# Kernel optimization log

Measured on AMD Instinct MI355X. Metric: run time of the kernel, lower is better.

Reference implementation:

```python
import jax, jax.numpy as jnp
import numpy as np

NUM_ENTITIES = 50000
NUM_RELATIONS = 500
DIM = 100
BATCH = 16
EPS = 1e-5  # torch BatchNorm1d default eps


def _bn2(x, gamma, beta):
    # train-mode BatchNorm1d on (B, d): stats over batch axis
    mean = jnp.mean(x, axis=0, keepdims=True)
    var = jnp.var(x, axis=0, keepdims=True)
    return (x - mean) * jax.lax.rsqrt(var + EPS) * gamma + beta


def _bn3(x, gamma, beta):
    # train-mode BatchNorm1d on (B, d, N): stats over (batch, length)
    mean = jnp.mean(x, axis=(0, 2), keepdims=True)
    var = jnp.var(x, axis=(0, 2), keepdims=True)
    return (x - mean) * jax.lax.rsqrt(var + EPS) * gamma[None, :, None] + beta[None, :, None]


def _cmul(a, b):
    return (a[0] * b[0] - a[1] * b[1], a[0] * b[1] + a[1] * b[0])


def _cadd(a, b):
    return (a[0] + b[0], a[1] + b[1])


def _cdiv(a, b):
    den = b[0] * b[0] + b[1] * b[1]
    return ((a[0] * b[0] + a[1] * b[1]) / den, (a[1] * b[0] - a[0] * b[1]) / den)


def setup_inputs() -> dict:
    key = jax.random.key(0)
    ks = jax.random.split(key, 12)
    d = DIM
    inp = {
        "h_idx": jax.random.randint(ks[0], (BATCH,), 0, NUM_ENTITIES),
        "r_idx": jax.random.randint(ks[1], (BATCH,), 0, NUM_RELATIONS),
        # ComplexEmbedding E (real, imag)
        "E_a": jax.random.normal(ks[2], (NUM_ENTITIES, d), jnp.float32) * 0.1,
        "E_b": jax.random.normal(ks[3], (NUM_ENTITIES, d), jnp.float32) * 0.1,
        # MobiusEmbedding R: 4 complex coefficients (a,b,c,d), real/imag parts
        "R_re": jax.random.normal(ks[4], (NUM_RELATIONS, 4, d), jnp.float32) * 0.1,
        "R_im": jax.random.normal(ks[5], (NUM_RELATIONS, 4, d), jnp.float32) * 0.1,
        # plain relation embedding feeding the Tucker cores
        "R2": jax.random.normal(ks[6], (NUM_RELATIONS, d), jnp.float32) * 0.1,
        # Tucker cores (relation_dim, entity_dim, entity_dim)
        "W_re": jax.random.uniform(ks[7], (d, d, d), jnp.float32, -0.1, 0.1),
        "W_im": jax.random.uniform(ks[8], (d, d, d), jnp.float32, -0.1, 0.1),
    }
    # BatchNorm affine params (bn0/bn1 of each CoreTuckER, and complex E_bn)
    gk = jax.random.split(ks[9], 6)
    bk = jax.random.split(ks[10], 6)
    names = ["g0r", "g1r", "g0i", "g1i", "gEa", "gEb"]
    bnames = ["b0r", "b1r", "b0i", "b1i", "bEa", "bEb"]
    for i, (gn, bn) in enumerate(zip(names, bnames)):
        inp[gn] = 1.0 + 0.05 * jax.random.normal(gk[i], (d,), jnp.float32)
        inp[bn] = 0.05 * jax.random.normal(bk[i], (d,), jnp.float32)
    return inp


def _forward(h_idx, r_idx, E_a, E_b, R_re, R_im, R2, W_re, W_im,
             g0r, b0r, g1r, b1r, g0i, b0i, g1i, b1i, gEa, bEa, gEb, bEb):
    h_a = E_a[h_idx]            # (B, d)
    h_b = E_b[h_idx]
    r2 = R2[r_idx]              # (B, d)

    # relation-specific Tucker maps W_mat = r2 . W  -> (B, d, d)
    Wm_re = jnp.einsum("bk,kef->bef", r2, W_re)
    Wm_im = jnp.einsum("bk,kef->bef", r2, W_im)

    def core(h, Wm, g0, b0, g1, b1):
        x = _bn2(h, g0, b0)
        x = jnp.einsum("be,bef->bf", x, Wm)  # (B,1,d) bmm (B,d,d)
        return _bn2(x, g1, b1)

    t_a = core(h_a, Wm_re, g0r, b0r, g1r, b1r)
    t_b = core(h_b, Wm_im, g0i, b0i, g1i, b1i)

    # Mobius multiplication: (h*r_a + r_b) / (h*r_c + r_d)
    rr = R_re[r_idx]            # (B, 4, d)
    ri = R_im[r_idx]
    h = (t_a, t_b)
    r_a = (rr[:, 0], ri[:, 0]); r_b = (rr[:, 1], ri[:, 1])
    r_c = (rr[:, 2], ri[:, 2]); r_d = (rr[:, 3], ri[:, 3])
    top = _cadd(_cmul(h, r_a), r_b)
    bot = _cadd(_cmul(h, r_c), r_d)
    t = _cdiv(top, bot)         # complex pair, each (B, d)

    # transform ALL entities with the same relation-specific Tucker map
    # CoreTuckER.w: (B,e,f) x (N,e) -> (B, f, N)
    Ea_t = jnp.einsum("bef,ne->bfn", Wm_re, E_a)
    Eb_t = jnp.einsum("bef,ne->bfn", Wm_im, E_b)
    # ComplexBatchNorm1d on (B, d, N); dropout is identity in eval mode
    Ea_t = _bn3(Ea_t, gEa, bEa)
    Eb_t = _bn3(Eb_t, gEb, bEb)

    # BatchComplexScoringAll: (B,1,d) bmm (B,d,N) for each complex part
    score = (jnp.einsum("bf,bfn->bn", t[0], Ea_t)
             + jnp.einsum("bf,bfn->bn", t[1], Eb_t))
    return jax.nn.sigmoid(score)  # (B, N)


def reference(h_idx, r_idx, E_a, E_b, R_re, R_im, R2, W_re, W_im,
              g0r, b0r, g1r, b1r, g0i, b0i, g1i, b1i, gEa, bEa, gEb, bEb):
    return _forward(h_idx, r_idx, E_a, E_b, R_re, R_im, R2, W_re, W_im,
                    g0r, b0r, g1r, b1r, g0i, b0i, g1i, b1i, gEa, bEa, gEb, bEb)
```

## Files before the change

### kernel.cpp

```cpp
#include <hip/hip_runtime.h>
#include <math.h>

#define D100 100
#define NE 50000
#define BATCH 16
#define EPS_F 1e-5f
#define TPT 782
#define NB2 196
#define TPB2 4
#define SLICES 16
#define QCI 10
#define QNJ 1664

typedef __attribute__((ext_vector_type(8))) short short8;
typedef __attribute__((ext_vector_type(16))) float float16;
typedef unsigned short u16;

__device__ __forceinline__ u16 f2bf(float x) {
  union { float f; unsigned u; } c; c.f = x;
  unsigned r = c.u + 0x7FFFu + ((c.u >> 16) & 1u);
  return (u16)(r >> 16);
}
__device__ __forceinline__ float bf2f(u16 v) {
  return __uint_as_float(((unsigned)v) << 16);
}
__device__ __forceinline__ float f4get(const float4& v, int j) {
  switch (j) { case 0: return v.x; case 1: return v.y; case 2: return v.z; default: return v.w; }
}

__global__ void k1_wm(const float* __restrict__ W_re, const float* __restrict__ W_im,
                      const float* __restrict__ R2, const int* __restrict__ r_idx,
                      float* __restrict__ Wm) {
  const int t = blockIdx.y;
  const float* W = t ? W_im : W_re;
  int ef = blockIdx.x * 256 + threadIdx.x;
  if (ef >= 10000) return;
  int ridx[16];
#pragma unroll
  for (int b = 0; b < 16; b++) ridx[b] = r_idx[b];
  float acc[16];
#pragma unroll
  for (int b = 0; b < 16; b++) acc[b] = 0.f;
  for (int k = 0; k < 100; k++) {
    float w = W[k * 10000 + ef];
#pragma unroll
    for (int b = 0; b < 16; b++) acc[b] = fmaf(R2[ridx[b] * 100 + k], w, acc[b]);
  }
  float* o = Wm + t * 160000 + ef;
#pragma unroll
  for (int b = 0; b < 16; b++) o[b * 10000] = acc[b];
}

__global__ void k1a_wm(const float* __restrict__ W_re, const float* __restrict__ W_im,
                       const float* __restrict__ R2, const int* __restrict__ r_idx,
                       float* __restrict__ Wm_p) {
  const int t = blockIdx.z, kc = blockIdx.y;
  const float* W = t ? W_im : W_re;
  const float4* W4 = (const float4*)W;
  __shared__ float r2s[16][12];
  const int tid = threadIdx.x;
  for (int i = tid; i < 160; i += 256) {
    int b = i / 10, kk = i - b * 10;
    r2s[b][kk] = R2[r_idx[b] * 100 + kc * 10 + kk];
  }
  __syncthreads();
  int ef4 = blockIdx.x * 256 + tid;
  if (ef4 < 2500) {
    float4 acc[16];
#pragma unroll
    for (int b = 0; b < 16; b++) acc[b] = make_float4(0.f, 0.f, 0.f, 0.f);
#pragma unroll
    for (int kk = 0; kk < 10; kk++) {
      float4 w = W4[(kc * 10 + kk) * 2500 + ef4];
#pragma unroll
      for (int b = 0; b < 16; b++) {
        float r = r2s[b][kk];
        acc[b].x = fmaf(r, w.x, acc[b].x);
        acc[b].y = fmaf(r, w.y, acc[b].y);
        acc[b].z = fmaf(r, w.z, acc[b].z);
        acc[b].w = fmaf(r, w.w, acc[b].w);
      }
    }
    float4* o = (float4*)(Wm_p + (long)kc * 320000 + t * 160000);
#pragma unroll
    for (int b = 0; b < 16; b++) o[b * 2500 + ef4] = acc[b];
  }
}

__global__ void k1b_reduce(const float* __restrict__ Wm_p, float* __restrict__ Wm) {
  int i4 = blockIdx.x * 256 + threadIdx.x;
  if (i4 >= 80000) return;
  const float4* P4 = (const float4*)Wm_p;
  float4 o = make_float4(0.f, 0.f, 0.f, 0.f);
#pragma unroll
  for (int j = 0; j < 10; j++) {
    float4 a = P4[(long)j * 80000 + i4];
    o.x += a.x; o.y += a.y; o.z += a.z; o.w += a.w;
  }
  ((float4*)Wm)[i4] = o;
}

__global__ __launch_bounds__(256) void k2f_gram(const float* __restrict__ E_a,
                                                const float* __restrict__ E_b,
                                                float* __restrict__ Gp,
                                                float* __restrict__ CSp) {
  const int t = blockIdx.y, bx = blockIdx.x;
  const float4* E4 = (const float4*)(t ? E_b : E_a);
  __shared__ __align__(16) u16 FRl[4][4][512];
  const int tid = threadIdx.x;
  const int wave = tid >> 6, lane = tid & 63, l31 = lane & 31;

  for (int i = tid; i < 8192; i += 256) ((u16*)FRl)[i] = 0;

  const int ti0 = bx * TPB2;
  const int nt = min(ti0 + TPB2, TPT) - ti0;

  float16 acc0, acc1, acc2, acc3;
#pragma unroll 16
  for (int r = 0; r < 16; r++) { acc0[r] = 0.f; acc1[r] = 0.f; acc2[r] = 0.f; acc3[r] = 0.f; }
  float cs = 0.f;
  float4 st[7];

#define K2F_LOAD(tile)                                          \
  { int n0 = (tile) * 64;                                       \
    _Pragma("unroll")                                           \
    for (int s = 0; s < 7; s++) {                               \
      int i = s * 256 + tid;                                    \
      float4 v = make_float4(0.f, 0.f, 0.f, 0.f);               \
      if (i < 1600) {                                           \
        int nl = i / 25, e4 = i - nl * 25;                      \
        int n = n0 + nl;                                        \
        if (n < NE) v = E4[(long)n * 25 + e4];                  \
      }                                                         \
      st[s] = v;                                                \
    } }

#define K2F_WRITE()                                             \
  { _Pragma("unroll")                                           \
    for (int s = 0; s < 7; s++) {                               \
      int i = s * 256 + tid;                                    \
      if (i < 1600) {                                           \
        int nl = i / 25, e4 = i - nl * 25;                      \
        int half = (nl >> 3) & 1, ncl = nl >> 4, elem = nl & 7; \
        _Pragma("unroll")                                       \
        for (int j = 0; j < 4; j++) {                           \
          int e = e4 * 4 + j;                                   \
          FRl[e >> 5][ncl][((e & 31) + 32 * half) * 8 + elem] = f2bf(f4get(st[s], j)); \
        } } } }

  __syncthreads();
  K2F_LOAD(ti0);
  K2F_WRITE();
  __syncthreads();

  for (int tt = 0; tt < nt; tt++) {
    if (tt + 1 < nt) K2F_LOAD(ti0 + tt + 1);
#pragma unroll
    for (int ncl = 0; ncl < 4; ncl++) {
      const u16* pf = &FRl[0][ncl][lane * 8];
      short8 f0 = *(const short8*)pf;
      short8 f1 = *(const short8*)(pf + 2048);
      short8 f2 = *(const short8*)(pf + 4096);
      short8 f3 = *(const short8*)(pf + 6144);
      short8 av = *(const short8*)(pf + wave * 2048);
      acc0 = __builtin_amdgcn_mfma_f32_32x32x16_bf16(av, f0, acc0, 0, 0, 0);
      acc1 = __builtin_amdgcn_mfma_f32_32x32x16_bf16(av, f1, acc1, 0, 0, 0);
      acc2 = __builtin_amdgcn_mfma_f32_32x32x16_bf16(av, f2, acc2, 0, 0, 0);
      acc3 = __builtin_amdgcn_mfma_f32_32x32x16_bf16(av, f3, acc3, 0, 0, 0);
#pragma unroll
      for (int j = 0; j < 8; j++) cs += bf2f((u16)av[j]);
    }
    __syncthreads();
    if (tt + 1 < nt) K2F_WRITE();
    __syncthreads();
  }

  float* gp = Gp + ((long)t * NB2 + bx) * 10000;
#pragma unroll 16
  for (int r = 0; r < 16; r++) {
    int m = (r & 3) + 8 * (r >> 2) + 4 * (lane >> 5);
    int e = wave * 32 + m;
    if (e < 100) {
      gp[e * 100 + l31] = acc0[r];
      gp[e * 100 + 32 + l31] = acc1[r];
      gp[e * 100 + 64 + l31] = acc2[r];
      if (l31 < 4) gp[e * 100 + 96 + l31] = acc3[r];
    }
  }
  cs += __shfl_xor(cs, 32);
  int row = wave * 32 + l31;
  if (lane < 32 && row < 100)
    CSp[((long)t * NB2 + bx) * 100 + row] = cs;
}

__global__ __launch_bounds__(256, 4) void k2_gram(const float* __restrict__ E_a,
                                                  const float* __restrict__ E_b,
                                                  float* __restrict__ Gp,
                                                  float* __restrict__ CSp,
                                                  int NB, int RPB) {
  const int t = blockIdx.y;
  const float* E = t ? E_b : E_a;
  const float4* E4 = (const float4*)E;
  __shared__ float sm[32][128];
  const int tid = threadIdx.x;
  const int bx = blockIdx.x;
  int r0 = bx * RPB;
  int rend = min(r0 + RPB, NE);
  for (int i = tid; i < 32 * 28; i += 256) {
    int r = i / 28;
    sm[r][100 + (i - r * 28)] = 0.f;
  }
  float acc[8][8];
#pragma unroll
  for (int i = 0; i < 8; i++)
#pragma unroll
    for (int j = 0; j < 8; j++) acc[i][j] = 0.f;
  float cs = 0.f;
  const int ty = tid >> 4, tx = tid & 15;
  for (int base = r0; base < rend; base += 32) {
    int cnt = min(32, rend - base);
    __syncthreads();
    for (int i = tid; i < 800; i += 256) {
      int r = i / 25, c4 = i - r * 25;
      float4 v = make_float4(0.f, 0.f, 0.f, 0.f);
      if (r < cnt) v = E4[(long)(base + r) * 25 + c4];
      *(float4*)&sm[r][c4 * 4] = v;
    }
    __syncthreads();
#pragma unroll 2
    for (int r = 0; r < 32; r++) {
      float4 a0 = *(const float4*)&sm[r][ty * 8];
      float4 a1 = *(const float4*)&sm[r][ty * 8 + 4];
      float4 b0 = *(const float4*)&sm[r][tx * 8];
      float4 b1 = *(const float4*)&sm[r][tx * 8 + 4];
      float av[8] = {a0.x, a0.y, a0.z, a0.w, a1.x, a1.y, a1.z, a1.w};
      float bv[8] = {b0.x, b0.y, b0.z, b0.w, b1.x, b1.y, b1.z, b1.w};
#pragma unroll
      for (int i = 0; i < 8; i++)
#pragma unroll
        for (int j = 0; j < 8; j++) acc[i][j] = fmaf(av[i], bv[j], acc[i][j]);
    }
    if (tid < 100) {
#pragma unroll 4
      for (int r = 0; r < 32; r++) cs += sm[r][tid];
    }
  }
  float* gp = Gp + ((long)t * NB + bx) * 10000;
#pragma unroll
  for (int i = 0; i < 8; i++) {
    int e = ty * 8 + i;
    if (e < 100) {
#pragma unroll
      for (int j = 0; j < 8; j++) {
        int ep = tx * 8 + j;
        if (ep < 100) gp[e * 100 + ep] = acc[i][j];
      }
    }
  }
  if (tid < 100) CSp[((long)t * NB + bx) * 100 + tid] = cs;
}

__global__ void k3a_reduce(const float* __restrict__ Gp, const float* __restrict__ CSp,
                           float* __restrict__ Gp2, float* __restrict__ CSp2,
                           int NB, int seg) {
  int chunk = blockIdx.x, slice = blockIdx.y, t = blockIdx.z;
  int nb0 = slice * seg;
  int nb1 = min(nb0 + seg, NB);
  int idx = chunk * 256 + threadIdx.x;
  if (idx < 10000) {
    float s = 0.f;
    const float* p = Gp + ((long)t * NB + nb0) * 10000 + idx;
    for (int nb = nb0; nb < nb1; nb++, p += 10000) s += *p;
    Gp2[(t * SLICES + slice) * 10000 + idx] = s;
  }
  if (chunk == 0 && threadIdx.x < 100) {
    float s = 0.f;
    const float* p = CSp + ((long)t * NB + nb0) * 100 + threadIdx.x;
    for (int nb = nb0; nb < nb1; nb++, p += 100) s += *p;
    CSp2[(t * SLICES + slice) * 100 + threadIdx.x] = s;
  }
}

__global__ void k3b_reduce(const float* __restrict__ Gp2, const float* __restrict__ CSp2,
                           float* __restrict__ G, float* __restrict__ CS) {
  int chunk = blockIdx.x, t = blockIdx.y;
  int idx = chunk * 256 + threadIdx.x;
  if (idx < 10000) {
    float s = 0.f;
    const float* p = Gp2 + (long)t * SLICES * 10000 + idx;
#pragma unroll
    for (int sl = 0; sl < SLICES; sl++) s += p[sl * 10000];
    G[t * 10000 + idx] = s;
  }
  if (chunk == 0 && threadIdx.x < 100) {
    float s = 0.f;
    const float* p = CSp2 + (long)t * SLICES * 100 + threadIdx.x;
#pragma unroll
    for (int sl = 0; sl < SLICES; sl++) s += p[sl * 100];
    CS[t * 100 + threadIdx.x] = s;
  }
}

__global__ __launch_bounds__(128) void k6g_qf(const float* __restrict__ Wm,
                                              const float* __restrict__ G,
                                              const float* __restrict__ CS,
                                              float* __restrict__ qf,
                                              float* __restrict__ s2q) {
  const int cx = blockIdx.x, ci = blockIdx.y, t = blockIdx.z;
  const int tid = threadIdx.x;
  __shared__ float Gl[QCI][100];
  __shared__ float CSl[QCI];
  for (int i = tid; i < QCI * 100; i += 128) {
    int k = i / 100, e = i - k * 100;
    Gl[k][e] = G[t * 10000 + (ci * QCI + k) * 100 + e];
  }
  if (tid < QCI) CSl[tid] = CS[t * 100 + ci * QCI + tid];
  __syncthreads();
  int j = cx * 128 + tid;
  if (j >= 1600) return;
  int b = j / 100, f = j - b * 100;
  const float* Y = Wm + t * 160000 + b * 10000 + f;
  float yci[QCI];
  float cs2 = 0.f;
#pragma unroll
  for (int k = 0; k < QCI; k++) {
    yci[k] = Y[(ci * QCI + k) * 100];
    cs2 = fmaf(CSl[k], yci[k], cs2);
  }
  float acc = 0.f;
#pragma unroll 4
  for (int e = 0; e < 100; e++) {
    float ye = Y[e * 100];
    float i0 = 0.f, i1 = 0.f;
#pragma unroll
    for (int k = 0; k < QCI; k += 2) {
      i0 = fmaf(Gl[k][e], yci[k], i0);
      i1 = fmaf(Gl[k + 1][e], yci[k + 1], i1);
    }
    acc = fmaf(i0 + i1, ye, acc);
  }
  qf[((long)t * QCI + ci) * QNJ + j] = acc;
  s2q[((long)t * QCI + ci) * QNJ + j] = cs2;
}

__global__ __launch_bounds__(128) void k4a_traw(const float* __restrict__ E_a,
                                                const float* __restrict__ E_b,
                                                const int* __restrict__ h_idx,
                                                const float* __restrict__ Wm,
                                                const float* __restrict__ g0r, const float* __restrict__ b0r,
                                                const float* __restrict__ g0i, const float* __restrict__ b0i,
                                                const float* __restrict__ qf,
                                                const float* __restrict__ s2q,
                                                float* __restrict__ traw,
                                                float* __restrict__ s1pp,
                                                float* __restrict__ s2pp) {
  int bid = blockIdx.x;
  int t = bid >> 4, b = bid & 15;
  const float4* E4 = (const float4*)(t ? E_b : E_a);
  const float* g0 = t ? g0i : g0r;
  const float* be0 = t ? b0i : b0r;
  __shared__ float hrows[1600], x[100];
  int tid = threadIdx.x;
  for (int i = tid; i < 400; i += 128) {
    int b2 = i / 25, e4 = i - b2 * 25;
    float4 v = E4[(long)h_idx[b2] * 25 + e4];
    *(float4*)&hrows[b2 * 100 + e4 * 4] = v;
  }
  __syncthreads();
  if (tid < 100) {
    float m = 0.f, s = 0.f;
#pragma unroll
    for (int b2 = 0; b2 < 16; b2++) { float v = hrows[b2 * 100 + tid]; m += v; s += v * v; }
    m *= (1.f / 16.f);
    float var = s * (1.f / 16.f) - m * m;
    x[tid] = (hrows[b * 100 + tid] - m) * rsqrtf(var + EPS_F) * g0[tid] + be0[tid];
  }
  __syncthreads();
  if (tid < 100) {
    const float* W = Wm + t * 160000 + b * 10000 + tid;
    float s = 0.f;
    for (int e = 0; e < 100; e++) s = fmaf(x[e], W[e * 100], s);
    traw[t * 1600 + b * 100 + tid] = s;
    float s1 = 0.f, s2 = 0.f;
    const float* pq = qf + (long)t * QCI * QNJ + b * 100 + tid;
    const float* ps = s2q + (long)t * QCI * QNJ + b * 100 + tid;
#pragma unroll
    for (int ci = 0; ci < QCI; ci++) {
      s1 += pq[ci * QNJ];
      s2 += ps[ci * QNJ];
    }
    s1pp[t * 1600 + b * 100 + tid] = s1;
    s2pp[t * 1600 + b * 100 + tid] = s2;
  }
}

__global__ __launch_bounds__(256) void k4b_mid(const float* __restrict__ traw,
                                               const int* __restrict__ r_idx,
                                               const float* __restrict__ g1r, const float* __restrict__ b1r,
                                               const float* __restrict__ g1i, const float* __restrict__ b1i,
                                               const float* __restrict__ R_re, const float* __restrict__ R_im,
                                               const float* __restrict__ s1pp, const float* __restrict__ s2pp,
                                               const float* __restrict__ gEa, const float* __restrict__ bEa,
                                               const float* __restrict__ gEb, const float* __restrict__ bEb,
                                               float* __restrict__ w01, float* __restrict__ c) {
  int tid = threadIdx.x;
  __shared__ float tr[3200], t01l[3200];
  __shared__ float sca[200], shl[200], al[200], be[200];
  for (int i = tid; i < 3200; i += 256) tr[i] = traw[i];
  __syncthreads();
  if (tid < 200) {
    int tt = tid / 100, f = tid - tt * 100;
    float m = 0.f, s = 0.f;
#pragma unroll
    for (int b = 0; b < 16; b++) { float v = tr[tt * 1600 + b * 100 + f]; m += v; s += v * v; }
    m *= (1.f / 16.f);
    float var = s * (1.f / 16.f) - m * m;
    float g = tt ? g1i[f] : g1r[f];
    float bb = tt ? b1i[f] : b1r[f];
    float sc = rsqrtf(var + EPS_F) * g;
    sca[tid] = sc; shl[tid] = bb - m * sc;
    float s1 = 0.f, s2 = 0.f;
#pragma unroll
    for (int b2 = 0; b2 < 16; b2++) {
      s1 += s1pp[tt * 1600 + b2 * 100 + f];
      s2 += s2pp[tt * 1600 + b2 * 100 + f];
    }
    float mean = s2 * (1.f / 800000.f);
    float var2 = s1 * (1.f / 800000.f) - mean * mean;
    float gE = tt ? gEb[f] : gEa[f];
    float bE = tt ? bEb[f] : bEa[f];
    float aa = rsqrtf(var2 + EPS_F) * gE;
    al[tid] = aa; be[tid] = bE - mean * aa;
  }
  __syncthreads();
  for (int i = tid; i < 1600; i += 256) {
    int b = i / 100, f = i - b * 100;
    float va = tr[b * 100 + f] * sca[f] + shl[f];
    float vb = tr[1600 + b * 100 + f] * sca[100 + f] + shl[100 + f];
    int base = r_idx[b] * 400 + f;
    float ra0 = R_re[base],       ra1 = R_im[base];
    float rb0 = R_re[base + 100], rb1 = R_im[base + 100];
    float rc0 = R_re[base + 200], rc1 = R_im[base + 200];
    float rd0 = R_re[base + 300], rd1 = R_im[base + 300];
    float top0 = va * ra0 - vb * ra1 + rb0;
    float top1 = va * ra1 + vb * ra0 + rb1;
    float bot0 = va * rc0 - vb * rc1 + rd0;
    float bot1 = va * rc1 + vb * rc0 + rd1;
    float den = bot0 * bot0 + bot1 * bot1;
    float t0 = (top0 * bot0 + top1 * bot1) / den;
    float t1 = (top1 * bot0 - top0 * bot1) / den;
    t01l[i] = t0; t01l[1600 + i] = t1;
    w01[i] = t0 * al[f];
    w01[1600 + i] = t1 * al[100 + f];
  }
  __syncthreads();
  if (tid < 16) {
    float cc = 0.f;
    for (int f = 0; f < 100; f++) {
      cc += t01l[tid * 100 + f] * be[f] + t01l[1600 + tid * 100 + f] * be[100 + f];
    }
    c[tid] = cc;
  }
}

__global__ __launch_bounds__(256) void k4c_u(const float* __restrict__ Wm,
                                             const float* __restrict__ w01,
                                             float* __restrict__ u) {
  int bid = blockIdx.x;
  int t = bid >> 4, b = bid & 15;
  __shared__ float w[100];
  __shared__ float Wl[100 * 101];
  int tid = threadIdx.x;
  if (tid < 100) w[tid] = w01[t * 1600 + b * 100 + tid];
  const float4* W4 = (const float4*)(Wm + t * 160000 + b * 10000);
  for (int i = tid; i < 2500; i += 256) {
    float4 v = W4[i];
    int e = (i * 4) / 100, f0 = (i * 4) - e * 100;
    float* dst = &Wl[e * 101 + f0];
    dst[0] = v.x; dst[1] = v.y; dst[2] = v.z; dst[3] = v.w;
  }
  __syncthreads();
  if (tid < 100) {
    const float* row = &Wl[tid * 101];
    float s = 0.f;
    for (int f = 0; f < 100; f++) s = fmaf(w[f], row[f], s);
    u[(t * 100 + tid) * 16 + b] = s;
  }
}

__global__ __launch_bounds__(256) void k9_score(const float* __restrict__ E_a,
                                                const float* __restrict__ E_b,
                                                const float* __restrict__ u,
                                                const float* __restrict__ c,
                                                float* __restrict__ out) {
  int n = blockIdx.x * 256 + threadIdx.x;
  if (n >= NE) return;
  const float4* Ea4 = (const float4*)E_a;
  const float4* Eb4 = (const float4*)E_b;
  float acc[16];
#pragma unroll
  for (int b = 0; b < 16; b++) acc[b] = 0.f;
  for (int e4 = 0; e4 < 25; e4++) {
    float4 va = Ea4[n * 25 + e4];
    float4 vb = Eb4[n * 25 + e4];
    const float* ua = u + e4 * 64;
    const float* ub = u + 1600 + e4 * 64;
#pragma unroll
    for (int j = 0; j < 4; j++) {
      float fa = f4get(va, j);
      float fb = f4get(vb, j);
#pragma unroll
      for (int b = 0; b < 16; b++) {
        acc[b] = fmaf(ua[j * 16 + b], fa, acc[b]);
        acc[b] = fmaf(ub[j * 16 + b], fb, acc[b]);
      }
    }
  }
#pragma unroll
  for (int b = 0; b < 16; b++) {
    float x = acc[b] + c[b];
    out[b * NE + n] = 1.f / (1.f + expf(-x));
  }
}

extern "C" void kernel_launch(void* const* d_in, const int* in_sizes, int n_in,
                              void* d_out, int out_size, void* d_ws, size_t ws_size,
                              hipStream_t stream) {
  const int* h_idx = (const int*)d_in[0];
  const int* r_idx = (const int*)d_in[1];
  const float* E_a = (const float*)d_in[2];
  const float* E_b = (const float*)d_in[3];
  const float* R_re = (const float*)d_in[4];
  const float* R_im = (const float*)d_in[5];
  const float* R2 = (const float*)d_in[6];
  const float* W_re = (const float*)d_in[7];
  const float* W_im = (const float*)d_in[8];
  const float* g0r = (const float*)d_in[9];
  const float* b0r = (const float*)d_in[10];
  const float* g1r = (const float*)d_in[11];
  const float* b1r = (const float*)d_in[12];
  const float* g0i = (const float*)d_in[13];
  const float* b0i = (const float*)d_in[14];
  const float* g1i = (const float*)d_in[15];
  const float* b1i = (const float*)d_in[16];
  const float* gEa = (const float*)d_in[17];
  const float* bEa = (const float*)d_in[18];
  const float* gEb = (const float*)d_in[19];
  const float* bEb = (const float*)d_in[20];
  float* out = (float*)d_out;
  float* ws = (float*)d_ws;

  float* Wm = ws;
  float* G = Wm + 320000;
  float* CS = G + 20000;
  float* u = CS + 200;
  float* c = u + 3200;
  float* qf = c + 16;
  float* s2q = qf + 33280;
  float* traw = s2q + 33280;
  float* w01 = traw + 3200;
  float* s1pp = w01 + 3200;
  float* s2pp = s1pp + 3200;
  const long fixed = 422776;

  float* un = ws + fixed;
  long avail = (long)(ws_size / 4);
  long unionFloats = avail - fixed - 64;

  float* Wm_p = un;
  int splitK1 = (unionFloats >= 3200000);
  if (splitK1) {
    hipLaunchKernelGGL(k1a_wm, dim3(10, 10, 2), dim3(256), 0, stream, W_re, W_im, R2, r_idx, Wm_p);
    hipLaunchKernelGGL(k1b_reduce, dim3(313), dim3(256), 0, stream, Wm_p, Wm);
  } else {
    hipLaunchKernelGGL(k1_wm, dim3(40, 2), dim3(256), 0, stream, W_re, W_im, R2, r_idx, Wm);
  }

  const long needMain = 323200 + (long)NB2 * 20200;
  if (unionFloats >= needMain) {
    float* Gp2 = un;
    float* CSp2 = Gp2 + 320000;
    float* Gp = CSp2 + 3200;
    float* CSp = Gp + (long)NB2 * 20000;
    int seg = (NB2 + SLICES - 1) / SLICES;
    hipLaunchKernelGGL(k2f_gram, dim3(NB2, 2), dim3(256), 0, stream, E_a, E_b, Gp, CSp);
    hipLaunchKernelGGL(k3a_reduce, dim3(40, SLICES, 2), dim3(256), 0, stream,
                       Gp, CSp, Gp2, CSp2, NB2, seg);
    hipLaunchKernelGGL(k3b_reduce, dim3(40, 2), dim3(256), 0, stream, Gp2, CSp2, G, CS);
  } else {
    float* Gp2 = un;
    float* CSp2 = Gp2 + 320000;
    float* Gp = CSp2 + 3200;
    long room = (unionFloats - 323200) / 20200;
    int NB = room < 360 ? (int)room : 360;
    if (NB < 1) NB = 1;
    int RPB = (NE + NB - 1) / NB;
    int seg = (NB + SLICES - 1) / SLICES;
    float* CSp = Gp + (long)NB * 20000;
    hipLaunchKernelGGL(k2_gram, dim3(NB, 2), dim3(256), 0, stream, E_a, E_b, Gp, CSp, NB, RPB);
    hipLaunchKernelGGL(k3a_reduce, dim3(40, SLICES, 2), dim3(256), 0, stream,
                       Gp, CSp, Gp2, CSp2, NB, seg);
    hipLaunchKernelGGL(k3b_reduce, dim3(40, 2), dim3(256), 0, stream, Gp2, CSp2, G, CS);
  }

  hipLaunchKernelGGL(k6g_qf, dim3(13, QCI, 2), dim3(128), 0, stream, Wm, G, CS, qf, s2q);
  hipLaunchKernelGGL(k4a_traw, dim3(32), dim3(128), 0, stream, E_a, E_b, h_idx, Wm,
                     g0r, b0r, g0i, b0i, qf, s2q, traw, s1pp, s2pp);
  hipLaunchKernelGGL(k4b_mid, dim3(1), dim3(256), 0, stream, traw, r_idx,
                     g1r, b1r, g1i, b1i, R_re, R_im, s1pp, s2pp,
                     gEa, bEa, gEb, bEb, w01, c);
  hipLaunchKernelGGL(k4c_u, dim3(32), dim3(256), 0, stream, Wm, w01, u);
  hipLaunchKernelGGL(k9_score, dim3((NE + 255) / 256), dim3(256), 0, stream,
                     E_a, E_b, u, c, out);
}
```

Before: 97.13 us.

## Merge pipeline into fewer fused kernels and run Wm with the Gram pass

The Wm contraction now runs as extra blocks inside the Gram MFMA kernel (kA) instead of in separate launches. The two-stage partial-Gram reduction becomes a single pass fused with the head-row BatchNorm/traw computation (kB). The qf and midstream kernels are restructured into a per-batch kD that also computes u. Gram tiles per block double, halving the partial count. The aim is to cut launch count and serial dependency overhead, at the cost of less parallel reductions and redundant per-block statistics work in kD.

Result: slower. 126.1 us (+29.8%).

```diff
diff --git a/kernel.cpp b/kernel.cpp
--- a/kernel.cpp
+++ b/kernel.cpp
@@ -6,10 +6,10 @@
 #define BATCH 16
 #define EPS_F 1e-5f
 #define TPT 782
-#define NB2 196
-#define TPB2 4
-#define SLICES 16
-#define QCI 10
+#define TPB2 8
+#define NBG 98
+#define QCI 20
+#define QCB 5
 #define QNJ 1664
 
 typedef __attribute__((ext_vector_type(8))) short short8;
@@ -28,169 +28,132 @@
   switch (j) { case 0: return v.x; case 1: return v.y; case 2: return v.z; default: return v.w; }
 }
 
-__global__ void k1_wm(const float* __restrict__ W_re, const float* __restrict__ W_im,
-                      const float* __restrict__ R2, const int* __restrict__ r_idx,
-                      float* __restrict__ Wm) {
-  const int t = blockIdx.y;
-  const float* W = t ? W_im : W_re;
-  int ef = blockIdx.x * 256 + threadIdx.x;
-  if (ef >= 10000) return;
-  int ridx[16];
-#pragma unroll
-  for (int b = 0; b < 16; b++) ridx[b] = r_idx[b];
-  float acc[16];
-#pragma unroll
-  for (int b = 0; b < 16; b++) acc[b] = 0.f;
-  for (int k = 0; k < 100; k++) {
-    float w = W[k * 10000 + ef];
-#pragma unroll
-    for (int b = 0; b < 16; b++) acc[b] = fmaf(R2[ridx[b] * 100 + k], w, acc[b]);
-  }
-  float* o = Wm + t * 160000 + ef;
-#pragma unroll
-  for (int b = 0; b < 16; b++) o[b * 10000] = acc[b];
-}
-
-__global__ void k1a_wm(const float* __restrict__ W_re, const float* __restrict__ W_im,
-                       const float* __restrict__ R2, const int* __restrict__ r_idx,
-                       float* __restrict__ Wm_p) {
-  const int t = blockIdx.z, kc = blockIdx.y;
-  const float* W = t ? W_im : W_re;
-  const float4* W4 = (const float4*)W;
-  __shared__ float r2s[16][12];
-  const int tid = threadIdx.x;
-  for (int i = tid; i < 160; i += 256) {
-    int b = i / 10, kk = i - b * 10;
-    r2s[b][kk] = R2[r_idx[b] * 100 + kc * 10 + kk];
-  }
-  __syncthreads();
-  int ef4 = blockIdx.x * 256 + tid;
-  if (ef4 < 2500) {
-    float4 acc[16];
-#pragma unroll
-    for (int b = 0; b < 16; b++) acc[b] = make_float4(0.f, 0.f, 0.f, 0.f);
-#pragma unroll
-    for (int kk = 0; kk < 10; kk++) {
-      float4 w = W4[(kc * 10 + kk) * 2500 + ef4];
-#pragma unroll
-      for (int b = 0; b < 16; b++) {
-        float r = r2s[b][kk];
-        acc[b].x = fmaf(r, w.x, acc[b].x);
-        acc[b].y = fmaf(r, w.y, acc[b].y);
-        acc[b].z = fmaf(r, w.z, acc[b].z);
-        acc[b].w = fmaf(r, w.w, acc[b].w);
-      }
-    }
-    float4* o = (float4*)(Wm_p + (long)kc * 320000 + t * 160000);
-#pragma unroll
-    for (int b = 0; b < 16; b++) o[b * 2500 + ef4] = acc[b];
-  }
-}
-
-__global__ void k1b_reduce(const float* __restrict__ Wm_p, float* __restrict__ Wm) {
-  int i4 = blockIdx.x * 256 + threadIdx.x;
-  if (i4 >= 80000) return;
-  const float4* P4 = (const float4*)Wm_p;
-  float4 o = make_float4(0.f, 0.f, 0.f, 0.f);
-#pragma unroll
-  for (int j = 0; j < 10; j++) {
-    float4 a = P4[(long)j * 80000 + i4];
-    o.x += a.x; o.y += a.y; o.z += a.z; o.w += a.w;
-  }
-  ((float4*)Wm)[i4] = o;
-}
-
-__global__ __launch_bounds__(256) void k2f_gram(const float* __restrict__ E_a,
-                                                const float* __restrict__ E_b,
-                                                float* __restrict__ Gp,
-                                                float* __restrict__ CSp) {
-  const int t = blockIdx.y, bx = blockIdx.x;
-  const float4* E4 = (const float4*)(t ? E_b : E_a);
-  __shared__ __align__(16) u16 FRl[4][4][512];
-  const int tid = threadIdx.x;
-  const int wave = tid >> 6, lane = tid & 63, l31 = lane & 31;
-
-  for (int i = tid; i < 8192; i += 256) ((u16*)FRl)[i] = 0;
-
-  const int ti0 = bx * TPB2;
-  const int nt = min(ti0 + TPB2, TPT) - ti0;
-
-  float16 acc0, acc1, acc2, acc3;
+__global__ __launch_bounds__(256) void kA(const float* __restrict__ W_re,
+                                          const float* __restrict__ W_im,
+                                          const float* __restrict__ R2,
+                                          const int* __restrict__ r_idx,
+                                          const float* __restrict__ E_a,
+                                          const float* __restrict__ E_b,
+                                          float* __restrict__ Wm,
+                                          float* __restrict__ Gp,
+                                          float* __restrict__ CSp,
+                                          int nbg) {
+  __shared__ __align__(16) u16 smem[8192];
+  const int bid = blockIdx.x, tid = threadIdx.x;
+
+  if (bid < 2 * nbg) {
+    const int t = bid / nbg, bx = bid - t * nbg;
+    const float4* E4 = (const float4*)(t ? E_b : E_a);
+    u16* FR = smem;
+    const int wave = tid >> 6, lane = tid & 63, l31 = lane & 31;
+
+    for (int i = tid; i < 8192; i += 256) FR[i] = 0;
+
+    const int ti0 = bx * TPB2;
+    const int nt = min(ti0 + TPB2, TPT) - ti0;
+
+    float16 acc0, acc1, acc2, acc3;
 #pragma unroll 16
-  for (int r = 0; r < 16; r++) { acc0[r] = 0.f; acc1[r] = 0.f; acc2[r] = 0.f; acc3[r] = 0.f; }
-  float cs = 0.f;
-  float4 st[7];
+    for (int r = 0; r < 16; r++) { acc0[r] = 0.f; acc1[r] = 0.f; acc2[r] = 0.f; acc3[r] = 0.f; }
+    float cs = 0.f;
+    float4 st[7];
 
 #define K2F_LOAD(tile)                                          \
-  { int n0 = (tile) * 64;                                       \
-    _Pragma("unroll")                                           \
-    for (int s = 0; s < 7; s++) {                               \
-      int i = s * 256 + tid;                                    \
-      float4 v = make_float4(0.f, 0.f, 0.f, 0.f);               \
-      if (i < 1600) {                                           \
-        int nl = i / 25, e4 = i - nl * 25;                      \
-        int n = n0 + nl;                                        \
-        if (n < NE) v = E4[(long)n * 25 + e4];                  \
-      }                                                         \
-      st[s] = v;                                                \
-    } }
+    { int n0 = (tile) * 64;                                     \
+      _Pragma("unroll")                                         \
+      for (int s = 0; s < 7; s++) {                             \
+        int i = s * 256 + tid;                                  \
+        float4 v = make_float4(0.f, 0.f, 0.f, 0.f);             \
+        if (i < 1600) {                                         \
+          int nl = i / 25, e4 = i - nl * 25;                    \
+          int n = n0 + nl;                                      \
+          if (n < NE) v = E4[(long)n * 25 + e4];                \
+        }                                                       \
+        st[s] = v;                                              \
+      } }
 
 #define K2F_WRITE()                                             \
-  { _Pragma("unroll")                                           \
-    for (int s = 0; s < 7; s++) {                               \
-      int i = s * 256 + tid;                                    \
-      if (i < 1600) {                                           \
-        int nl = i / 25, e4 = i - nl * 25;                      \
-        int half = (nl >> 3) & 1, ncl = nl >> 4, elem = nl & 7; \
-        _Pragma("unroll")                                       \
-        for (int j = 0; j < 4; j++) {                           \
-          int e = e4 * 4 + j;                                   \
-          FRl[e >> 5][ncl][((e & 31) + 32 * half) * 8 + elem] = f2bf(f4get(st[s], j)); \
-        } } } }
-
-  __syncthreads();
-  K2F_LOAD(ti0);
-  K2F_WRITE();
-  __syncthreads();
-
-  for (int tt = 0; tt < nt; tt++) {
-    if (tt + 1 < nt) K2F_LOAD(ti0 + tt + 1);
-#pragma unroll
-    for (int ncl = 0; ncl < 4; ncl++) {
-      const u16* pf = &FRl[0][ncl][lane * 8];
-      short8 f0 = *(const short8*)pf;
-      short8 f1 = *(const short8*)(pf + 2048);
-      short8 f2 = *(const short8*)(pf + 4096);
-      short8 f3 = *(const short8*)(pf + 6144);
-      short8 av = *(const short8*)(pf + wave * 2048);
-      acc0 = __builtin_amdgcn_mfma_f32_32x32x16_bf16(av, f0, acc0, 0, 0, 0);
-      acc1 = __builtin_amdgcn_mfma_f32_32x32x16_bf16(av, f1, acc1, 0, 0, 0);
-      acc2 = __builtin_amdgcn_mfma_f32_32x32x16_bf16(av, f2, acc2, 0, 0, 0);
-      acc3 = __builtin_amdgcn_mfma_f32_32x32x16_bf16(av, f3, acc3, 0, 0, 0);
-#pragma unroll
-      for (int j = 0; j < 8; j++) cs += bf2f((u16)av[j]);
-    }
-    __syncthreads();
-    if (tt + 1 < nt) K2F_WRITE();
-    __syncthreads();
-  }
-
-  float* gp = Gp + ((long)t * NB2 + bx) * 10000;
+    { _Pragma("unroll")                                         \
+      for (int s = 0; s < 7; s++) {                             \
+        int i = s * 256 + tid;                                  \
+        if (i < 1600) {                                         \
+          int nl = i / 25, e4 = i - nl * 25;                    \
+          int half = (nl >> 3) & 1, ncl = nl >> 4, elem = nl & 7; \
+          _Pragma("unroll")                                     \
+          for (int j = 0; j < 4; j++) {                         \
+            int e = e4 * 4 + j;                                 \
+            FR[(e >> 5) * 2048 + ncl * 512 + ((e & 31) + 32 * half) * 8 + elem] = f2bf(f4get(st[s], j)); \
+          } } } }
+
+    __syncthreads();
+    K2F_LOAD(ti0);
+    K2F_WRITE();
+    __syncthreads();
+
+    for (int tt = 0; tt < nt; tt++) {
+      if (tt + 1 < nt) K2F_LOAD(ti0 + tt + 1);
+#pragma unroll
+      for (int ncl = 0; ncl < 4; ncl++) {
+        const u16* pf = FR + ncl * 512 + lane * 8;
+        short8 f0 = *(const short8*)pf;
+        short8 f1 = *(const short8*)(pf + 2048);
+        short8 f2 = *(const short8*)(pf + 4096);
+        short8 f3 = *(const short8*)(pf + 6144);
+        short8 av = *(const short8*)(pf + wave * 2048);
+        acc0 = __builtin_amdgcn_mfma_f32_32x32x16_bf16(av, f0, acc0, 0, 0, 0);
+        acc1 = __builtin_amdgcn_mfma_f32_32x32x16_bf16(av, f1, acc1, 0, 0, 0);
+        acc2 = __builtin_amdgcn_mfma_f32_32x32x16_bf16(av, f2, acc2, 0, 0, 0);
+        acc3 = __builtin_amdgcn_mfma_f32_32x32x16_bf16(av, f3, acc3, 0, 0, 0);
+#pragma unroll
+        for (int j = 0; j < 8; j++) cs += bf2f((u16)av[j]);
+      }
+      __syncthreads();
+      if (tt + 1 < nt) {
+        K2F_WRITE();
+        __syncthreads();
+      }
+    }
+
+    float* gp = Gp + ((long)t * NBG + bx) * 10000;
 #pragma unroll 16
-  for (int r = 0; r < 16; r++) {
-    int m = (r & 3) + 8 * (r >> 2) + 4 * (lane >> 5);
-    int e = wave * 32 + m;
-    if (e < 100) {
-      gp[e * 100 + l31] = acc0[r];
-      gp[e * 100 + 32 + l31] = acc1[r];
-      gp[e * 100 + 64 + l31] = acc2[r];
-      if (l31 < 4) gp[e * 100 + 96 + l31] = acc3[r];
-    }
-  }
-  cs += __shfl_xor(cs, 32);
-  int row = wave * 32 + l31;
-  if (lane < 32 && row < 100)
-    CSp[((long)t * NB2 + bx) * 100 + row] = cs;
+    for (int r = 0; r < 16; r++) {
+      int m = (r & 3) + 8 * (r >> 2) + 4 * (lane >> 5);
+      int e = wave * 32 + m;
+      if (e < 100) {
+        gp[e * 100 + l31] = acc0[r];
+        gp[e * 100 + 32 + l31] = acc1[r];
+        gp[e * 100 + 64 + l31] = acc2[r];
+        if (l31 < 4) gp[e * 100 + 96 + l31] = acc3[r];
+      }
+    }
+    cs += __shfl_xor(cs, 32);
+    int row = wave * 32 + l31;
+    if (lane < 32 && row < 100)
+      CSp[((long)t * NBG + bx) * 100 + row] = cs;
+  } else {
+    int bid2 = bid - 2 * nbg;
+    int t = bid2 / 40, bx = bid2 - t * 40;
+    const float* W = t ? W_im : W_re;
+    int ridx[16];
+#pragma unroll
+    for (int b = 0; b < 16; b++) ridx[b] = r_idx[b];
+    int ef = bx * 256 + tid;
+    if (ef < 10000) {
+      float acc[16];
+#pragma unroll
+      for (int b = 0; b < 16; b++) acc[b] = 0.f;
+      const float* wp = W + ef;
+#pragma unroll 4
+      for (int k = 0; k < 100; k++) {
+        float w = wp[k * 10000];
+#pragma unroll
+        for (int b = 0; b < 16; b++) acc[b] = fmaf(R2[ridx[b] * 100 + k], w, acc[b]);
+      }
+      float* o = Wm + t * 160000 + ef;
+#pragma unroll
+      for (int b = 0; b < 16; b++) o[b * 10000] = acc[b];
+    }
+  }
 }
 
 __global__ __launch_bounds__(256, 4) void k2_gram(const float* __restrict__ E_a,
@@ -260,55 +223,76 @@
   if (tid < 100) CSp[((long)t * NB + bx) * 100 + tid] = cs;
 }
 
-__global__ void k3a_reduce(const float* __restrict__ Gp, const float* __restrict__ CSp,
-                           float* __restrict__ Gp2, float* __restrict__ CSp2,
-                           int NB, int seg) {
-  int chunk = blockIdx.x, slice = blockIdx.y, t = blockIdx.z;
-  int nb0 = slice * seg;
-  int nb1 = min(nb0 + seg, NB);
-  int idx = chunk * 256 + threadIdx.x;
-  if (idx < 10000) {
-    float s = 0.f;
-    const float* p = Gp + ((long)t * NB + nb0) * 10000 + idx;
-    for (int nb = nb0; nb < nb1; nb++, p += 10000) s += *p;
-    Gp2[(t * SLICES + slice) * 10000 + idx] = s;
-  }
-  if (chunk == 0 && threadIdx.x < 100) {
-    float s = 0.f;
-    const float* p = CSp + ((long)t * NB + nb0) * 100 + threadIdx.x;
-    for (int nb = nb0; nb < nb1; nb++, p += 100) s += *p;
-    CSp2[(t * SLICES + slice) * 100 + threadIdx.x] = s;
-  }
-}
-
-__global__ void k3b_reduce(const float* __restrict__ Gp2, const float* __restrict__ CSp2,
-                           float* __restrict__ G, float* __restrict__ CS) {
-  int chunk = blockIdx.x, t = blockIdx.y;
-  int idx = chunk * 256 + threadIdx.x;
-  if (idx < 10000) {
-    float s = 0.f;
-    const float* p = Gp2 + (long)t * SLICES * 10000 + idx;
-#pragma unroll
-    for (int sl = 0; sl < SLICES; sl++) s += p[sl * 10000];
-    G[t * 10000 + idx] = s;
-  }
-  if (chunk == 0 && threadIdx.x < 100) {
-    float s = 0.f;
-    const float* p = CSp2 + (long)t * SLICES * 100 + threadIdx.x;
-#pragma unroll
-    for (int sl = 0; sl < SLICES; sl++) s += p[sl * 100];
-    CS[t * 100 + threadIdx.x] = s;
-  }
-}
-
-__global__ __launch_bounds__(128) void k6g_qf(const float* __restrict__ Wm,
-                                              const float* __restrict__ G,
-                                              const float* __restrict__ CS,
-                                              float* __restrict__ qf,
-                                              float* __restrict__ s2q) {
-  const int cx = blockIdx.x, ci = blockIdx.y, t = blockIdx.z;
+__global__ __launch_bounds__(256) void kB(const float* __restrict__ Gp,
+                                          const float* __restrict__ CSp,
+                                          float* __restrict__ G,
+                                          float* __restrict__ CS,
+                                          int NB,
+                                          const float* __restrict__ E_a,
+                                          const float* __restrict__ E_b,
+                                          const int* __restrict__ h_idx,
+                                          const float* __restrict__ Wm,
+                                          const float* __restrict__ g0r, const float* __restrict__ b0r,
+                                          const float* __restrict__ g0i, const float* __restrict__ b0i,
+                                          float* __restrict__ traw) {
+  __shared__ float hrows[1600], x[100];
+  const int bid = blockIdx.x, tid = threadIdx.x;
+  if (bid < 80) {
+    int t = bid / 40, chunk = bid - t * 40;
+    int idx = chunk * 256 + tid;
+    if (idx < 10000) {
+      float s = 0.f;
+      const float* p = Gp + (long)t * NB * 10000 + idx;
+#pragma unroll 2
+      for (int nb = 0; nb < NB; nb++, p += 10000) s += *p;
+      G[t * 10000 + idx] = s;
+    }
+    if (chunk == 0 && tid < 100) {
+      float s = 0.f;
+      const float* p = CSp + (long)t * NB * 100 + tid;
+      for (int nb = 0; nb < NB; nb++, p += 100) s += *p;
+      CS[t * 100 + tid] = s;
+    }
+  } else {
+    int bid2 = bid - 80;
+    int t = bid2 >> 4, b = bid2 & 15;
+    const float4* E4 = (const float4*)(t ? E_b : E_a);
+    const float* g0 = t ? g0i : g0r;
+    const float* be0 = t ? b0i : b0r;
+    for (int i = tid; i < 400; i += 256) {
+      int b2 = i / 25, e4 = i - b2 * 25;
+      float4 v = E4[(long)h_idx[b2] * 25 + e4];
+      *(float4*)&hrows[b2 * 100 + e4 * 4] = v;
+    }
+    __syncthreads();
+    if (tid < 100) {
+      float m = 0.f, s = 0.f;
+#pragma unroll
+      for (int b2 = 0; b2 < 16; b2++) { float v = hrows[b2 * 100 + tid]; m += v; s += v * v; }
+      m *= (1.f / 16.f);
+      float var = s * (1.f / 16.f) - m * m;
+      x[tid] = (hrows[b * 100 + tid] - m) * rsqrtf(var + EPS_F) * g0[tid] + be0[tid];
+    }
+    __syncthreads();
+    if (tid < 100) {
+      const float* W = Wm + t * 160000 + b * 10000 + tid;
+      float s = 0.f;
+#pragma unroll 4
+      for (int e = 0; e < 100; e++) s = fmaf(x[e], W[e * 100], s);
+      traw[t * 1600 + b * 100 + tid] = s;
+    }
+  }
+}
+
+__global__ __launch_bounds__(128) void kC(const float* __restrict__ Wm,
+                                          const float* __restrict__ G,
+                                          const float* __restrict__ CS,
+                                          float* __restrict__ qf,
+                                          float* __restrict__ s2q) {
+  const int bid = blockIdx.x;
+  const int cx = bid % 13, ci = (bid / 13) % QCB, t = bid / (13 * QCB);
   const int tid = threadIdx.x;
-  __shared__ float Gl[QCI][100];
+  __shared__ __align__(16) float Gl[QCI][100];
   __shared__ float CSl[QCI];
   for (int i = tid; i < QCI * 100; i += 128) {
     int k = i / 100, e = i - k * 100;
@@ -328,84 +312,41 @@
     cs2 = fmaf(CSl[k], yci[k], cs2);
   }
   float acc = 0.f;
-#pragma unroll 4
-  for (int e = 0; e < 100; e++) {
-    float ye = Y[e * 100];
-    float i0 = 0.f, i1 = 0.f;
-#pragma unroll
-    for (int k = 0; k < QCI; k += 2) {
-      i0 = fmaf(Gl[k][e], yci[k], i0);
-      i1 = fmaf(Gl[k + 1][e], yci[k + 1], i1);
-    }
-    acc = fmaf(i0 + i1, ye, acc);
-  }
-  qf[((long)t * QCI + ci) * QNJ + j] = acc;
-  s2q[((long)t * QCI + ci) * QNJ + j] = cs2;
-}
-
-__global__ __launch_bounds__(128) void k4a_traw(const float* __restrict__ E_a,
-                                                const float* __restrict__ E_b,
-                                                const int* __restrict__ h_idx,
-                                                const float* __restrict__ Wm,
-                                                const float* __restrict__ g0r, const float* __restrict__ b0r,
-                                                const float* __restrict__ g0i, const float* __restrict__ b0i,
-                                                const float* __restrict__ qf,
-                                                const float* __restrict__ s2q,
-                                                float* __restrict__ traw,
-                                                float* __restrict__ s1pp,
-                                                float* __restrict__ s2pp) {
-  int bid = blockIdx.x;
-  int t = bid >> 4, b = bid & 15;
-  const float4* E4 = (const float4*)(t ? E_b : E_a);
-  const float* g0 = t ? g0i : g0r;
-  const float* be0 = t ? b0i : b0r;
-  __shared__ float hrows[1600], x[100];
-  int tid = threadIdx.x;
-  for (int i = tid; i < 400; i += 128) {
-    int b2 = i / 25, e4 = i - b2 * 25;
-    float4 v = E4[(long)h_idx[b2] * 25 + e4];
-    *(float4*)&hrows[b2 * 100 + e4 * 4] = v;
-  }
-  __syncthreads();
-  if (tid < 100) {
-    float m = 0.f, s = 0.f;
-#pragma unroll
-    for (int b2 = 0; b2 < 16; b2++) { float v = hrows[b2 * 100 + tid]; m += v; s += v * v; }
-    m *= (1.f / 16.f);
-    float var = s * (1.f / 16.f) - m * m;
-    x[tid] = (hrows[b * 100 + tid] - m) * rsqrtf(var + EPS_F) * g0[tid] + be0[tid];
-  }
-  __syncthreads();
-  if (tid < 100) {
-    const float* W = Wm + t * 160000 + b * 10000 + tid;
-    float s = 0.f;
-    for (int e = 0; e < 100; e++) s = fmaf(x[e], W[e * 100], s);
-    traw[t * 1600 + b * 100 + tid] = s;
-    float s1 = 0.f, s2 = 0.f;
-    const float* pq = qf + (long)t * QCI * QNJ + b * 100 + tid;
-    const float* ps = s2q + (long)t * QCI * QNJ + b * 100 + tid;
-#pragma unroll
-    for (int ci = 0; ci < QCI; ci++) {
-      s1 += pq[ci * QNJ];
-      s2 += ps[ci * QNJ];
-    }
-    s1pp[t * 1600 + b * 100 + tid] = s1;
-    s2pp[t * 1600 + b * 100 + tid] = s2;
-  }
-}
-
-__global__ __launch_bounds__(256) void k4b_mid(const float* __restrict__ traw,
-                                               const int* __restrict__ r_idx,
-                                               const float* __restrict__ g1r, const float* __restrict__ b1r,
-                                               const float* __restrict__ g1i, const float* __restrict__ b1i,
-                                               const float* __restrict__ R_re, const float* __restrict__ R_im,
-                                               const float* __restrict__ s1pp, const float* __restrict__ s2pp,
-                                               const float* __restrict__ gEa, const float* __restrict__ bEa,
-                                               const float* __restrict__ gEb, const float* __restrict__ bEb,
-                                               float* __restrict__ w01, float* __restrict__ c) {
-  int tid = threadIdx.x;
-  __shared__ float tr[3200], t01l[3200];
-  __shared__ float sca[200], shl[200], al[200], be[200];
+#pragma unroll 5
+  for (int e4 = 0; e4 < 25; e4++) {
+    float ye0 = Y[(e4 * 4 + 0) * 100];
+    float ye1 = Y[(e4 * 4 + 1) * 100];
+    float ye2 = Y[(e4 * 4 + 2) * 100];
+    float ye3 = Y[(e4 * 4 + 3) * 100];
+    float s0 = 0.f, s1 = 0.f, s2 = 0.f, s3 = 0.f;
+#pragma unroll
+    for (int k = 0; k < QCI; k++) {
+      float4 g = *(const float4*)&Gl[k][e4 * 4];
+      s0 = fmaf(g.x, yci[k], s0);
+      s1 = fmaf(g.y, yci[k], s1);
+      s2 = fmaf(g.z, yci[k], s2);
+      s3 = fmaf(g.w, yci[k], s3);
+    }
+    acc += s0 * ye0 + s1 * ye1 + s2 * ye2 + s3 * ye3;
+  }
+  qf[((long)t * QCB + ci) * QNJ + j] = acc;
+  s2q[((long)t * QCB + ci) * QNJ + j] = cs2;
+}
+
+__global__ __launch_bounds__(256) void kD(const float* __restrict__ traw,
+                                          const int* __restrict__ r_idx,
+                                          const float* __restrict__ g1r, const float* __restrict__ b1r,
+                                          const float* __restrict__ g1i, const float* __restrict__ b1i,
+                                          const float* __restrict__ R_re, const float* __restrict__ R_im,
+                                          const float* __restrict__ qf, const float* __restrict__ s2q,
+                                          const float* __restrict__ gEa, const float* __restrict__ bEa,
+                                          const float* __restrict__ gEb, const float* __restrict__ bEb,
+                                          const float* __restrict__ Wm,
+                                          float* __restrict__ u, float* __restrict__ c) {
+  const int bo = blockIdx.x, tid = threadIdx.x;
+  __shared__ float tr[3200], sca[200], shl[200], al[200], be[200];
+  __shared__ float w0[100], w1[100], t01l[200], pc[128];
+  __shared__ float Wl[10100];
   for (int i = tid; i < 3200; i += 256) tr[i] = traw[i];
   __syncthreads();
   if (tid < 200) {
@@ -420,10 +361,15 @@
     float sc = rsqrtf(var + EPS_F) * g;
     sca[tid] = sc; shl[tid] = bb - m * sc;
     float s1 = 0.f, s2 = 0.f;
-#pragma unroll
-    for (int b2 = 0; b2 < 16; b2++) {
-      s1 += s1pp[tt * 1600 + b2 * 100 + f];
-      s2 += s2pp[tt * 1600 + b2 * 100 + f];
+    const float* q = qf + (long)tt * QCB * QNJ + f;
+    const float* z = s2q + (long)tt * QCB * QNJ + f;
+#pragma unroll
+    for (int ci = 0; ci < QCB; ci++) {
+#pragma unroll
+      for (int b2 = 0; b2 < 16; b2++) {
+        s1 += q[ci * QNJ + b2 * 100];
+        s2 += z[ci * QNJ + b2 * 100];
+      }
     }
     float mean = s2 * (1.f / 800000.f);
     float var2 = s1 * (1.f / 800000.f) - mean * mean;
@@ -433,11 +379,11 @@
     al[tid] = aa; be[tid] = bE - mean * aa;
   }
   __syncthreads();
-  for (int i = tid; i < 1600; i += 256) {
-    int b = i / 100, f = i - b * 100;
-    float va = tr[b * 100 + f] * sca[f] + shl[f];
-    float vb = tr[1600 + b * 100 + f] * sca[100 + f] + shl[100 + f];
-    int base = r_idx[b] * 400 + f;
+  if (tid < 100) {
+    int f = tid;
+    float va = tr[bo * 100 + f] * sca[f] + shl[f];
+    float vb = tr[1600 + bo * 100 + f] * sca[100 + f] + shl[100 + f];
+    int base = r_idx[bo] * 400 + f;
     float ra0 = R_re[base],       ra1 = R_im[base];
     float rb0 = R_re[base + 100], rb1 = R_im[base + 100];
     float rc0 = R_re[base + 200], rc1 = R_im[base + 200];
@@ -449,42 +395,38 @@
     float den = bot0 * bot0 + bot1 * bot1;
     float t0 = (top0 * bot0 + top1 * bot1) / den;
     float t1 = (top1 * bot0 - top0 * bot1) / den;
-    t01l[i] = t0; t01l[1600 + i] = t1;
-    w01[i] = t0 * al[f];
-    w01[1600 + i] = t1 * al[100 + f];
-  }
+    t01l[f] = t0; t01l[100 + f] = t1;
+    w0[f] = t0 * al[f];
+    w1[f] = t1 * al[100 + f];
+  }
+  if (tid < 128) pc[tid] = 0.f;
   __syncthreads();
-  if (tid < 16) {
-    float cc = 0.f;
-    for (int f = 0; f < 100; f++) {
-      cc += t01l[tid * 100 + f] * be[f] + t01l[1600 + tid * 100 + f] * be[100 + f];
-    }
-    c[tid] = cc;
-  }
-}
-
-__global__ __launch_bounds__(256) void k4c_u(const float* __restrict__ Wm,
-                                             const float* __restrict__ w01,
-                                             float* __restrict__ u) {
-  int bid = blockIdx.x;
-  int t = bid >> 4, b = bid & 15;
-  __shared__ float w[100];
-  __shared__ float Wl[100 * 101];
-  int tid = threadIdx.x;
-  if (tid < 100) w[tid] = w01[t * 1600 + b * 100 + tid];
-  const float4* W4 = (const float4*)(Wm + t * 160000 + b * 10000);
-  for (int i = tid; i < 2500; i += 256) {
-    float4 v = W4[i];
-    int e = (i * 4) / 100, f0 = (i * 4) - e * 100;
-    float* dst = &Wl[e * 101 + f0];
-    dst[0] = v.x; dst[1] = v.y; dst[2] = v.z; dst[3] = v.w;
-  }
+  if (tid < 100) pc[tid] = t01l[tid] * be[tid] + t01l[100 + tid] * be[100 + tid];
   __syncthreads();
-  if (tid < 100) {
-    const float* row = &Wl[tid * 101];
-    float s = 0.f;
-    for (int f = 0; f < 100; f++) s = fmaf(w[f], row[f], s);
-    u[(t * 100 + tid) * 16 + b] = s;
+  for (int o = 64; o > 0; o >>= 1) {
+    if (tid < o) pc[tid] += pc[tid + o];
+    __syncthreads();
+  }
+  if (tid == 0) c[bo] = pc[0];
+#pragma unroll 2
+  for (int t = 0; t < 2; t++) {
+    __syncthreads();
+    const float4* W4 = (const float4*)(Wm + t * 160000 + bo * 10000);
+    for (int i = tid; i < 2500; i += 256) {
+      float4 v = W4[i];
+      int e = (i * 4) / 100, f0 = (i * 4) - e * 100;
+      float* dst = &Wl[e * 101 + f0];
+      dst[0] = v.x; dst[1] = v.y; dst[2] = v.z; dst[3] = v.w;
+    }
+    __syncthreads();
+    if (tid < 100) {
+      const float* row = &Wl[tid * 101];
+      const float* w = t ? w1 : w0;
+      float s = 0.f;
+#pragma unroll 4
+      for (int f = 0; f < 100; f++) s = fmaf(w[f], row[f], s);
+      u[(t * 100 + tid) * 16 + bo] = s;
+    }
   }
 }
 
@@ -556,60 +498,39 @@
   float* u = CS + 200;
   float* c = u + 3200;
   float* qf = c + 16;
-  float* s2q = qf + 33280;
-  float* traw = s2q + 33280;
-  float* w01 = traw + 3200;
-  float* s1pp = w01 + 3200;
-  float* s2pp = s1pp + 3200;
-  const long fixed = 422776;
+  float* s2q = qf + 16640;
+  float* traw = s2q + 16640;
+  const long fixed = 379896;
 
   float* un = ws + fixed;
   long avail = (long)(ws_size / 4);
   long unionFloats = avail - fixed - 64;
 
-  float* Wm_p = un;
-  int splitK1 = (unionFloats >= 3200000);
-  if (splitK1) {
-    hipLaunchKernelGGL(k1a_wm, dim3(10, 10, 2), dim3(256), 0, stream, W_re, W_im, R2, r_idx, Wm_p);
-    hipLaunchKernelGGL(k1b_reduce, dim3(313), dim3(256), 0, stream, Wm_p, Wm);
+  const long needMain = (long)NBG * 2 * 10000 + (long)NBG * 2 * 100;
+  int NB = NBG;
+  float* Gp = un;
+  float* CSp = Gp + (long)NB * 20000;
+
+  if (unionFloats >= needMain) {
+    hipLaunchKernelGGL(kA, dim3(2 * NBG + 80), dim3(256), 0, stream,
+                       W_re, W_im, R2, r_idx, E_a, E_b, Wm, Gp, CSp, NBG);
   } else {
-    hipLaunchKernelGGL(k1_wm, dim3(40, 2), dim3(256), 0, stream, W_re, W_im, R2, r_idx, Wm);
-  }
-
-  const long needMain = 323200 + (long)NB2 * 20200;
-  if (unionFloats >= needMain) {
-    float* Gp2 = un;
-    float* CSp2 = Gp2 + 320000;
-    float* Gp = CSp2 + 3200;
-    float* CSp = Gp + (long)NB2 * 20000;
-    int seg = (NB2 + SLICES - 1) / SLICES;
-    hipLaunchKernelGGL(k2f_gram, dim3(NB2, 2), dim3(256), 0, stream, E_a, E_b, Gp, CSp);
-    hipLaunchKernelGGL(k3a_reduce, dim3(40, SLICES, 2), dim3(256), 0, stream,
-                       Gp, CSp, Gp2, CSp2, NB2, seg);
-    hipLaunchKernelGGL(k3b_reduce, dim3(40, 2), dim3(256), 0, stream, Gp2, CSp2, G, CS);
-  } else {
-    float* Gp2 = un;
-    float* CSp2 = Gp2 + 320000;
-    float* Gp = CSp2 + 3200;
-    long room = (unionFloats - 323200) / 20200;
-    int NB = room < 360 ? (int)room : 360;
+    long room = (unionFloats) / 20200;
+    NB = room < NBG ? (int)room : NBG;
     if (NB < 1) NB = 1;
+    CSp = Gp + (long)NB * 20000;
     int RPB = (NE + NB - 1) / NB;
-    int seg = (NB + SLICES - 1) / SLICES;
-    float* CSp = Gp + (long)NB * 20000;
+    hipLaunchKernelGGL(kA, dim3(80), dim3(256), 0, stream,
+                       W_re, W_im, R2, r_idx, E_a, E_b, Wm, Gp, CSp, 0);
     hipLaunchKernelGGL(k2_gram, dim3(NB, 2), dim3(256), 0, stream, E_a, E_b, Gp, CSp, NB, RPB);
-    hipLaunchKernelGGL(k3a_reduce, dim3(40, SLICES, 2), dim3(256), 0, stream,
-                       Gp, CSp, Gp2, CSp2, NB, seg);
-    hipLaunchKernelGGL(k3b_reduce, dim3(40, 2), dim3(256), 0, stream, Gp2, CSp2, G, CS);
-  }
-
-  hipLaunchKernelGGL(k6g_qf, dim3(13, QCI, 2), dim3(128), 0, stream, Wm, G, CS, qf, s2q);
-  hipLaunchKernelGGL(k4a_traw, dim3(32), dim3(128), 0, stream, E_a, E_b, h_idx, Wm,
-                     g0r, b0r, g0i, b0i, qf, s2q, traw, s1pp, s2pp);
-  hipLaunchKernelGGL(k4b_mid, dim3(1), dim3(256), 0, stream, traw, r_idx,
-                     g1r, b1r, g1i, b1i, R_re, R_im, s1pp, s2pp,
-                     gEa, bEa, gEb, bEb, w01, c);
-  hipLaunchKernelGGL(k4c_u, dim3(32), dim3(256), 0, stream, Wm, w01, u);
+  }
+
+  hipLaunchKernelGGL(kB, dim3(112), dim3(256), 0, stream, Gp, CSp, G, CS, NB,
+                     E_a, E_b, h_idx, Wm, g0r, b0r, g0i, b0i, traw);
+  hipLaunchKernelGGL(kC, dim3(13 * QCB * 2), dim3(128), 0, stream, Wm, G, CS, qf, s2q);
+  hipLaunchKernelGGL(kD, dim3(16), dim3(256), 0, stream, traw, r_idx,
+                     g1r, b1r, g1i, b1i, R_re, R_im, qf, s2q,
+                     gEa, bEa, gEb, bEb, Wm, u, c);
   hipLaunchKernelGGL(k9_score, dim3((NE + 255) / 256), dim3(256), 0, stream,
                      E_a, E_b, u, c, out);
 }
```
